# Optimization experiments

Hardware: AMD Instinct MI355X
Metric: run time of the kernel (lower is better)

## Reference

```python
import jax, jax.numpy as jnp
import numpy as np

# opt hyperparameters
_S, _M, _N_PILOT, _K, _L, _DECAY = 6, 64, 1, 16, 8, 4.0
_N, _P = 4096, 4
_SMK = (_S + 1) * (_M + _N_PILOT + _K)  # 567


def _conv_full(a, b):
    # a: (B, L), b: (B, S) -> (B, S+L-1) full convolution per batch row
    return jax.vmap(lambda u, v: jnp.convolve(u, v, mode='full'))(a, b)


def setup_inputs() -> dict:
    key = jax.random.key(0)
    k1, k2 = jax.random.split(key)
    x = jax.random.normal(k1, (_N, _P, _SMK, 2), dtype=jnp.float32)
    # exponential power-delay profile, normalized (as in __init__/sample)
    power = jnp.exp(-jnp.arange(_L, dtype=jnp.float32) / _DECAY)
    power = power / jnp.sum(power)
    cof = jnp.sqrt(power / 2.0)[None, None, :, None] * jax.random.normal(
        k2, (_N, _P, _L, 2), dtype=jnp.float32)
    return {"x": x, "cof": cof, "M": _M}


def reference(x, cof, M):
    # x: (N,P,SMK,2) complex signal (re/im stacked), cof: (N,P,L,2) channel taps
    N, P, SMK, _ = x.shape
    L = cof.shape[2]
    B = N * P
    hr = cof[..., 0].reshape(B, L)
    hi = cof[..., 1].reshape(B, L)
    xr = x[..., 0].reshape(B, SMK)
    xi = x[..., 1].reshape(B, SMK)
    # complex FIR full convolution: out[i] = sum_j h[i-j] * x[j]
    out_r = _conv_full(hr, xr) - _conv_full(hi, xi)
    out_i = _conv_full(hr, xi) + _conv_full(hi, xr)
    out = jnp.stack([out_r, out_i], axis=-1).reshape(N, P, SMK + L - 1, 2)
    # frequency response: FFT of taps zero-padded to M
    cof_true = jnp.pad(cof, ((0, 0), (0, 0), (0, M - L), (0, 0)))
    Hc = jnp.fft.fft(cof_true[..., 0] + 1j * cof_true[..., 1], axis=-1)
    H_true = jnp.stack([Hc.real.astype(x.dtype), Hc.imag.astype(x.dtype)], axis=-1)
    return out, H_true
```

## Files before the change

### kernel.cpp

```cpp
#include <hip/hip_runtime.h>
#include <math.h>


#define B_ROWS 16384
#define SMK    567
#define LTAPS  8
#define OUTLEN 574
#define MFFT   64

__global__ __launch_bounds__(256) void channel_kernel(
    const float2* __restrict__ x,
    const float2* __restrict__ cof,
    float2* __restrict__ out,
    float2* __restrict__ H)
{
    __shared__ float2 xs[OUTLEN + LTAPS - 1];

    const int b   = blockIdx.x;
    const int tid = threadIdx.x;

    const float2* __restrict__ xrow = x + (size_t)b * SMK;

    if (tid < 2 * (LTAPS - 1)) {
        int idx = (tid < LTAPS - 1) ? tid : (OUTLEN + tid - (LTAPS - 1));
        xs[idx] = make_float2(0.0f, 0.0f);
    }
    for (int i = tid; i < SMK; i += 256) {
        xs[i + (LTAPS - 1)] = xrow[i];
    }

    const float2* __restrict__ crow = cof + (size_t)b * LTAPS;
    float2 h[LTAPS];
    #pragma unroll
    for (int j = 0; j < LTAPS; ++j) h[j] = crow[j];

    __syncthreads();

    float2* __restrict__ orow = out + (size_t)b * OUTLEN;
    #pragma unroll
    for (int it = 0; it < 3; ++it) {
        int i = tid + it * 256;
        if (i < OUTLEN) {
            float sr = 0.0f, si = 0.0f;
            #pragma unroll
            for (int j = 0; j < LTAPS; ++j) {
                float2 xv = xs[i - j + (LTAPS - 1)];
                sr = fmaf(h[j].x, xv.x, sr);
                sr = fmaf(-h[j].y, xv.y, sr);
                si = fmaf(h[j].x, xv.y, si);
                si = fmaf(h[j].y, xv.x, si);
            }
            orow[i] = make_float2(sr, si);
        }
    }

    if (tid < MFFT) {
        const int k = tid;
        float accr = 0.0f, acci = 0.0f;
        #pragma unroll
        for (int l = 0; l < LTAPS; ++l) {
            int t = (k * l) & (MFFT - 1);
            float ang = -6.2831853071795864769f * (float)t * (1.0f / (float)MFFT);
            float s, c;
            __sincosf(ang, &s, &c);
            accr = fmaf(h[l].x, c, accr);
            accr = fmaf(-h[l].y, s, accr);
            acci = fmaf(h[l].x, s, acci);
            acci = fmaf(h[l].y, c, acci);
        }
        H[(size_t)b * MFFT + k] = make_float2(accr, acci);
    }
}

extern "C" void kernel_launch(void* const* d_in, const int* in_sizes, int n_in,
                              void* d_out, int out_size, void* d_ws, size_t ws_size,
                              hipStream_t stream) {
    const float2* x   = (const float2*)d_in[0];
    const float2* cof = (const float2*)d_in[1];
    float* outf = (float*)d_out;

    float2* conv_out = (float2*)outf;
    float2* H        = (float2*)(outf + (size_t)B_ROWS * OUTLEN * 2);

    channel_kernel<<<B_ROWS, 256, 0, stream>>>(x, cof, conv_out, H);
}
```

Measured before the change: 29.67 us.

## Process two rows per block with float4 vectorized loads and stores

```diff
diff --git a/kernel.cpp b/kernel.cpp
--- a/kernel.cpp
+++ b/kernel.cpp
@@ -7,80 +7,105 @@
 #define LTAPS  8
 #define OUTLEN 574
 #define MFFT   64
+#define PADS   (LTAPS - 1)
+#define XSLEN  (SMK + 2 * PADS)
 
 __global__ __launch_bounds__(256) void channel_kernel(
-    const float2* __restrict__ x,
-    const float2* __restrict__ cof,
-    float2* __restrict__ out,
-    float2* __restrict__ H)
+    const float4* __restrict__ x4,
+    const float4* __restrict__ cof4,
+    float4* __restrict__ out4,
+    float4* __restrict__ H4)
 {
-    __shared__ float2 xs[OUTLEN + LTAPS - 1];
+    __shared__ float2 xs[2][XSLEN];
+    __shared__ float2 ht[2][LTAPS];
 
-    const int b   = blockIdx.x;
+    const int bid = blockIdx.x;
     const int tid = threadIdx.x;
 
-    const float2* __restrict__ xrow = x + (size_t)b * SMK;
-
-    if (tid < 2 * (LTAPS - 1)) {
-        int idx = (tid < LTAPS - 1) ? tid : (OUTLEN + tid - (LTAPS - 1));
-        xs[idx] = make_float2(0.0f, 0.0f);
-    }
-    for (int i = tid; i < SMK; i += 256) {
-        xs[i + (LTAPS - 1)] = xrow[i];
+    if (tid < 2 * 2 * PADS) {
+        int r = tid / (2 * PADS);
+        int p = tid % (2 * PADS);
+        int idx = (p < PADS) ? p : (SMK + p);
+        xs[r][idx] = make_float2(0.0f, 0.0f);
     }
 
-    const float2* __restrict__ crow = cof + (size_t)b * LTAPS;
-    float2 h[LTAPS];
-    #pragma unroll
-    for (int j = 0; j < LTAPS; ++j) h[j] = crow[j];
+    const float4* __restrict__ xg = x4 + (size_t)bid * SMK;
+    for (int t = tid; t < SMK; t += 256) {
+        float4 v = xg[t];
+        int e0 = 2 * t;
+        int e1 = 2 * t + 1;
+        if (e0 < SMK) xs[0][e0 + PADS]       = make_float2(v.x, v.y);
+        else          xs[1][e0 - SMK + PADS] = make_float2(v.x, v.y);
+        if (e1 < SMK) xs[0][e1 + PADS]       = make_float2(v.z, v.w);
+        else          xs[1][e1 - SMK + PADS] = make_float2(v.z, v.w);
+    }
+
+    if (tid < 8) {
+        float4 v = cof4[(size_t)bid * 8 + tid];
+        float2* hf = &ht[0][0];
+        hf[2 * tid]     = make_float2(v.x, v.y);
+        hf[2 * tid + 1] = make_float2(v.z, v.w);
+    }
 
     __syncthreads();
 
-    float2* __restrict__ orow = out + (size_t)b * OUTLEN;
+    float4* __restrict__ og = out4 + (size_t)bid * OUTLEN;
     #pragma unroll
     for (int it = 0; it < 3; ++it) {
-        int i = tid + it * 256;
-        if (i < OUTLEN) {
-            float sr = 0.0f, si = 0.0f;
+        int v = tid + it * 256;
+        if (v < OUTLEN) {
+            int r   = (v >= OUTLEN / 2) ? 1 : 0;
+            int idx = v - r * (OUTLEN / 2);
+            const float2* __restrict__ hs = ht[r];
+            const float2* __restrict__ xr = xs[r];
+            int i0 = 2 * idx;
+            float sr0 = 0.f, si0 = 0.f, sr1 = 0.f, si1 = 0.f;
             #pragma unroll
             for (int j = 0; j < LTAPS; ++j) {
-                float2 xv = xs[i - j + (LTAPS - 1)];
-                sr = fmaf(h[j].x, xv.x, sr);
-                sr = fmaf(-h[j].y, xv.y, sr);
-                si = fmaf(h[j].x, xv.y, si);
-                si = fmaf(h[j].y, xv.x, si);
+                float2 hj = hs[j];
+                float2 a  = xr[i0 - j + PADS];
+                float2 c  = xr[i0 + 1 - j + PADS];
+                sr0 = fmaf(hj.x, a.x, sr0); sr0 = fmaf(-hj.y, a.y, sr0);
+                si0 = fmaf(hj.x, a.y, si0); si0 = fmaf(hj.y, a.x, si0);
+                sr1 = fmaf(hj.x, c.x, sr1); sr1 = fmaf(-hj.y, c.y, sr1);
+                si1 = fmaf(hj.x, c.y, si1); si1 = fmaf(hj.y, c.x, si1);
             }
-            orow[i] = make_float2(sr, si);
+            og[v] = make_float4(sr0, si0, sr1, si1);
         }
     }
 
     if (tid < MFFT) {
-        const int k = tid;
-        float accr = 0.0f, acci = 0.0f;
+        int r  = tid >> 5;
+        int kp = tid & 31;
+        const float2* __restrict__ hs = ht[r];
+        float ar0 = 0.f, ai0 = 0.f, ar1 = 0.f, ai1 = 0.f;
+        int k0 = 2 * kp, k1 = 2 * kp + 1;
         #pragma unroll
         for (int l = 0; l < LTAPS; ++l) {
-            int t = (k * l) & (MFFT - 1);
-            float ang = -6.2831853071795864769f * (float)t * (1.0f / (float)MFFT);
-            float s, c;
-            __sincosf(ang, &s, &c);
-            accr = fmaf(h[l].x, c, accr);
-            accr = fmaf(-h[l].y, s, accr);
-            acci = fmaf(h[l].x, s, acci);
-            acci = fmaf(h[l].y, c, acci);
+            float2 hl = hs[l];
+            int t0 = (k0 * l) & (MFFT - 1);
+            int t1 = (k1 * l) & (MFFT - 1);
+            float s0, c0, s1, c1;
+            __sincosf(-6.2831853071795864769f * (float)t0 * (1.0f / (float)MFFT), &s0, &c0);
+            __sincosf(-6.2831853071795864769f * (float)t1 * (1.0f / (float)MFFT), &s1, &c1);
+            ar0 = fmaf(hl.x, c0, ar0); ar0 = fmaf(-hl.y, s0, ar0);
+            ai0 = fmaf(hl.x, s0, ai0); ai0 = fmaf(hl.y, c0, ai0);
+            ar1 = fmaf(hl.x, c1, ar1); ar1 = fmaf(-hl.y, s1, ar1);
+            ai1 = fmaf(hl.x, s1, ai1); ai1 = fmaf(hl.y, c1, ai1);
         }
-        H[(size_t)b * MFFT + k] = make_float2(accr, acci);
+        H4[(size_t)bid * MFFT + tid] = make_float4(ar0, ai0, ar1, ai1);
     }
 }
 
 extern "C" void kernel_launch(void* const* d_in, const int* in_sizes, int n_in,
                               void* d_out, int out_size, void* d_ws, size_t ws_size,
                               hipStream_t stream) {
-    const float2* x   = (const float2*)d_in[0];
-    const float2* cof = (const float2*)d_in[1];
+    const float4* x4   = (const float4*)d_in[0];
+    const float4* cof4 = (const float4*)d_in[1];
     float* outf = (float*)d_out;
 
-    float2* conv_out = (float2*)outf;
-    float2* H        = (float2*)(outf + (size_t)B_ROWS * OUTLEN * 2);
+    float4* out4 = (float4*)outf;
+    float4* H4   = (float4*)(outf + (size_t)B_ROWS * OUTLEN * 2);
 
-    channel_kernel<<<B_ROWS, 256, 0, stream>>>(x, cof, conv_out, H);
+    channel_kernel<<<B_ROWS / 2, 256, 0, stream>>>(x4, cof4, out4, H4);
 }
```

Result: slower. 32.55 us (+9.7%).

## Assign one wavefront per row and replace block barrier with wave-local waitcnt

Applied to the files above, without the earlier changes.

```diff
diff --git a/kernel.cpp b/kernel.cpp
--- a/kernel.cpp
+++ b/kernel.cpp
@@ -7,6 +7,8 @@
 #define LTAPS  8
 #define OUTLEN 574
 #define MFFT   64
+#define PADS   (LTAPS - 1)
+#define XSLEN  (OUTLEN + PADS)
 
 __global__ __launch_bounds__(256) void channel_kernel(
     const float2* __restrict__ x,
@@ -14,19 +16,21 @@
     float2* __restrict__ out,
     float2* __restrict__ H)
 {
-    __shared__ float2 xs[OUTLEN + LTAPS - 1];
+    __shared__ float2 xs[4][XSLEN];
 
-    const int b   = blockIdx.x;
-    const int tid = threadIdx.x;
+    const int wave = threadIdx.x >> 6;
+    const int lane = threadIdx.x & 63;
+    const int b    = blockIdx.x * 4 + wave;
 
+    float2* __restrict__ s = xs[wave];
     const float2* __restrict__ xrow = x + (size_t)b * SMK;
 
-    if (tid < 2 * (LTAPS - 1)) {
-        int idx = (tid < LTAPS - 1) ? tid : (OUTLEN + tid - (LTAPS - 1));
-        xs[idx] = make_float2(0.0f, 0.0f);
+    if (lane < 2 * PADS) {
+        int idx = (lane < PADS) ? lane : (OUTLEN + lane - PADS);
+        s[idx] = make_float2(0.0f, 0.0f);
     }
-    for (int i = tid; i < SMK; i += 256) {
-        xs[i + (LTAPS - 1)] = xrow[i];
+    for (int i = lane; i < SMK; i += 64) {
+        s[i + PADS] = xrow[i];
     }
 
     const float2* __restrict__ crow = cof + (size_t)b * LTAPS;
@@ -34,17 +38,17 @@
     #pragma unroll
     for (int j = 0; j < LTAPS; ++j) h[j] = crow[j];
 
-    __syncthreads();
+    asm volatile("s_waitcnt vmcnt(0) lgkmcnt(0)" ::: "memory");
 
     float2* __restrict__ orow = out + (size_t)b * OUTLEN;
     #pragma unroll
-    for (int it = 0; it < 3; ++it) {
-        int i = tid + it * 256;
+    for (int it = 0; it < 9; ++it) {
+        int i = lane + it * 64;
         if (i < OUTLEN) {
             float sr = 0.0f, si = 0.0f;
             #pragma unroll
             for (int j = 0; j < LTAPS; ++j) {
-                float2 xv = xs[i - j + (LTAPS - 1)];
+                float2 xv = s[i - j + PADS];
                 sr = fmaf(h[j].x, xv.x, sr);
                 sr = fmaf(-h[j].y, xv.y, sr);
                 si = fmaf(h[j].x, xv.y, si);
@@ -54,19 +58,19 @@
         }
     }
 
-    if (tid < MFFT) {
-        const int k = tid;
+    {
+        const int k = lane;
         float accr = 0.0f, acci = 0.0f;
         #pragma unroll
         for (int l = 0; l < LTAPS; ++l) {
             int t = (k * l) & (MFFT - 1);
             float ang = -6.2831853071795864769f * (float)t * (1.0f / (float)MFFT);
-            float s, c;
-            __sincosf(ang, &s, &c);
-            accr = fmaf(h[l].x, c, accr);
-            accr = fmaf(-h[l].y, s, accr);
-            acci = fmaf(h[l].x, s, acci);
-            acci = fmaf(h[l].y, c, acci);
+            float sn, cs;
+            __sincosf(ang, &sn, &cs);
+            accr = fmaf(h[l].x, cs, accr);
+            accr = fmaf(-h[l].y, sn, accr);
+            acci = fmaf(h[l].x, sn, acci);
+            acci = fmaf(h[l].y, cs, acci);
         }
         H[(size_t)b * MFFT + k] = make_float2(accr, acci);
     }
@@ -82,5 +86,5 @@
     float2* conv_out = (float2*)outf;
     float2* H        = (float2*)(outf + (size_t)B_ROWS * OUTLEN * 2);
 
-    channel_kernel<<<B_ROWS, 256, 0, stream>>>(x, cof, conv_out, H);
+    channel_kernel<<<B_ROWS / 4, 256, 0, stream>>>(x, cof, conv_out, H);
 }
```

After: 33.99 us. 14.6% more time.

## Make blocks persistent over eight rows with double-buffered register prefetch

Applied to the files above, without the earlier changes.

```diff
diff --git a/kernel.cpp b/kernel.cpp
--- a/kernel.cpp
+++ b/kernel.cpp
@@ -7,6 +7,9 @@
 #define LTAPS  8
 #define OUTLEN 574
 #define MFFT   64
+#define XSLEN  582
+#define GRID   2048
+#define RPB    8
 
 __global__ __launch_bounds__(256) void channel_kernel(
     const float2* __restrict__ x,
@@ -14,61 +17,94 @@
     float2* __restrict__ out,
     float2* __restrict__ H)
 {
-    __shared__ float2 xs[OUTLEN + LTAPS - 1];
+    __shared__ float2 xs[2][XSLEN];
+    __shared__ float2 hs[2][LTAPS];
 
-    const int b   = blockIdx.x;
     const int tid = threadIdx.x;
+    const int g   = blockIdx.x;
+    const bool has2 = (tid + 512) < SMK;
 
-    const float2* __restrict__ xrow = x + (size_t)b * SMK;
-
-    if (tid < 2 * (LTAPS - 1)) {
-        int idx = (tid < LTAPS - 1) ? tid : (OUTLEN + tid - (LTAPS - 1));
-        xs[idx] = make_float2(0.0f, 0.0f);
-    }
-    for (int i = tid; i < SMK; i += 256) {
-        xs[i + (LTAPS - 1)] = xrow[i];
+    if (tid < 30) {
+        int bsel = tid / 15, p = tid % 15;
+        int idx = (p < 8) ? p : (SMK + p);
+        xs[bsel][idx] = make_float2(0.0f, 0.0f);
     }
 
-    const float2* __restrict__ crow = cof + (size_t)b * LTAPS;
-    float2 h[LTAPS];
-    #pragma unroll
-    for (int j = 0; j < LTAPS; ++j) h[j] = crow[j];
-
+    {
+        const float2* __restrict__ xrow = x + (size_t)g * SMK;
+        float2 v0 = xrow[tid];
+        float2 v1 = xrow[tid + 256];
+        float2 v2 = has2 ? xrow[tid + 512] : make_float2(0.f, 0.f);
+        xs[0][8 + tid]       = v0;
+        xs[0][8 + tid + 256] = v1;
+        if (has2) xs[0][8 + tid + 512] = v2;
+        if (tid < LTAPS) hs[0][tid] = cof[(size_t)g * LTAPS + tid];
+    }
     __syncthreads();
 
-    float2* __restrict__ orow = out + (size_t)b * OUTLEN;
-    #pragma unroll
-    for (int it = 0; it < 3; ++it) {
-        int i = tid + it * 256;
-        if (i < OUTLEN) {
-            float sr = 0.0f, si = 0.0f;
+    int cur = 0;
+    for (int t = 0; t < RPB; ++t) {
+        const size_t row = (size_t)t * GRID + g;
+
+        float2 v0, v1, v2, hv;
+        if (t + 1 < RPB) {
+            const size_t nrow = (size_t)(t + 1) * GRID + g;
+            const float2* __restrict__ xn = x + nrow * SMK;
+            v0 = xn[tid];
+            v1 = xn[tid + 256];
+            if (has2) v2 = xn[tid + 512];
+            if (tid < LTAPS) hv = cof[nrow * LTAPS + tid];
+        }
+
+        const float2* __restrict__ s = xs[cur];
+        float2 h[LTAPS];
+        #pragma unroll
+        for (int j = 0; j < LTAPS; ++j) h[j] = hs[cur][j];
+
+        float2* __restrict__ orow = out + row * OUTLEN;
+        #pragma unroll
+        for (int it = 0; it < 3; ++it) {
+            int i = tid + it * 256;
+            if (i < OUTLEN) {
+                float sr = 0.0f, si = 0.0f;
+                #pragma unroll
+                for (int j = 0; j < LTAPS; ++j) {
+                    float2 xv = s[i - j + 8];
+                    sr = fmaf(h[j].x, xv.x, sr);
+                    sr = fmaf(-h[j].y, xv.y, sr);
+                    si = fmaf(h[j].x, xv.y, si);
+                    si = fmaf(h[j].y, xv.x, si);
+                }
+                orow[i] = make_float2(sr, si);
+            }
+        }
+
+        if (tid < MFFT) {
+            const int k = tid;
+            float accr = 0.0f, acci = 0.0f;
             #pragma unroll
-            for (int j = 0; j < LTAPS; ++j) {
-                float2 xv = xs[i - j + (LTAPS - 1)];
-                sr = fmaf(h[j].x, xv.x, sr);
-                sr = fmaf(-h[j].y, xv.y, sr);
-                si = fmaf(h[j].x, xv.y, si);
-                si = fmaf(h[j].y, xv.x, si);
+            for (int l = 0; l < LTAPS; ++l) {
+                int tt = (k * l) & (MFFT - 1);
+                float ang = -6.2831853071795864769f * (float)tt * (1.0f / (float)MFFT);
+                float sn, cs;
+                __sincosf(ang, &sn, &cs);
+                accr = fmaf(h[l].x, cs, accr);
+                accr = fmaf(-h[l].y, sn, accr);
+                acci = fmaf(h[l].x, sn, acci);
+                acci = fmaf(h[l].y, cs, acci);
             }
-            orow[i] = make_float2(sr, si);
+            H[row * MFFT + k] = make_float2(accr, acci);
         }
-    }
 
-    if (tid < MFFT) {
-        const int k = tid;
-        float accr = 0.0f, acci = 0.0f;
-        #pragma unroll
-        for (int l = 0; l < LTAPS; ++l) {
-            int t = (k * l) & (MFFT - 1);
-            float ang = -6.2831853071795864769f * (float)t * (1.0f / (float)MFFT);
-            float s, c;
-            __sincosf(ang, &s, &c);
-            accr = fmaf(h[l].x, c, accr);
-            accr = fmaf(-h[l].y, s, accr);
-            acci = fmaf(h[l].x, s, acci);
-            acci = fmaf(h[l].y, c, acci);
+        if (t + 1 < RPB) {
+            int nxt = cur ^ 1;
+            xs[nxt][8 + tid]       = v0;
+            xs[nxt][8 + tid + 256] = v1;
+            if (has2) xs[nxt][8 + tid + 512] = v2;
+            if (tid < LTAPS) hs[nxt][tid] = hv;
+            cur = nxt;
         }
-        H[(size_t)b * MFFT + k] = make_float2(accr, acci);
+        __syncthreads();
     }
 }
 
@@ -82,5 +118,5 @@
     float2* conv_out = (float2*)outf;
     float2* H        = (float2*)(outf + (size_t)B_ROWS * OUTLEN * 2);
 
-    channel_kernel<<<B_ROWS, 256, 0, stream>>>(x, cof, conv_out, H);
+    channel_kernel<<<GRID, 256, 0, stream>>>(x, cof, conv_out, H);
 }
```

After: 32.99 us. 1.11x slower.
